# Optimization experiments

Hardware: AMD Instinct MI355X
Metric: run time of the kernel (lower is better)

Reference implementation:

```python
import jax, jax.numpy as jnp
import numpy as np

V, D, H, B, S, K = 10000, 128, 512, 32, 512, 2  # vocab, emb, hidden, batch, seq, num_cells

def setup_inputs() -> dict:
    key = jax.random.key(0)
    ks = jax.random.split(key, 8)
    sc_d, sc_h = 1.0 / np.sqrt(D), 1.0 / np.sqrt(H)
    return {
        "x": jax.random.randint(ks[0], (B, S), 0, V),
        "emb_table": jax.random.normal(ks[1], (V, D), jnp.float32),
        "W_ih": jax.random.uniform(ks[2], (K, 4 * H, D), jnp.float32, -sc_d, sc_d),
        "W_hh": jax.random.uniform(ks[3], (K, 4 * H, H), jnp.float32, -sc_h, sc_h),
        "b_ih": jax.random.uniform(ks[4], (K, 4 * H), jnp.float32, -sc_h, sc_h),
        "b_hh": jax.random.uniform(ks[5], (K, 4 * H), jnp.float32, -sc_h, sc_h),
        "W_out": jax.random.uniform(ks[6], (V, H), jnp.float32, -sc_h, sc_h),
        "b_out": jax.random.uniform(ks[7], (V,), jnp.float32, -sc_h, sc_h),
    }

def _mlstm(x_ids_t, emb_t, W_ih, W_hh, b, h0, c0):
    # x_ids_t: (S,B) int, emb_t: (S,B,D). Two LSTMCells; token id parity picks the cell.
    def step(carry, inp):
        h, c = carry                       # (B,H) each
        xt, ids = inp                      # (B,D), (B,)
        gates = (jnp.einsum('bd,kgd->kbg', xt, W_ih)
                 + jnp.einsum('bh,kgh->kbg', h, W_hh)
                 + b[:, None, :])          # (K,B,4H)
        i, f, g, o = jnp.split(gates, 4, axis=-1)
        i, f, o = jax.nn.sigmoid(i), jax.nn.sigmoid(f), jax.nn.sigmoid(o)
        g = jnp.tanh(g)
        c_new = f * c + i * g              # (K,B,H)
        h_new = o * jnp.tanh(c_new)        # (K,B,H)
        sel = (ids % 2)[:, None]           # (B,1) cell index per example
        h_next = jnp.where(sel == 0, h_new[0], h_new[1])
        c_next = jnp.where(sel == 0, c_new[0], c_new[1])
        return (h_next, c_next), h_next
    (_, _), hs = jax.lax.scan(step, (h0, c0), (emb_t, x_ids_t))
    return hs  # (S,B,H)

def reference(x, emb_table, W_ih, W_hh, b_ih, b_hh, W_out, b_out):
    emb = emb_table[x]                     # (B,S,D)
    emb_t = jnp.transpose(emb, (1, 0, 2))  # (S,B,D) time-major
    h0 = jnp.zeros((x.shape[0], W_hh.shape[-1]), emb.dtype)
    hs = _mlstm(x.T, emb_t, W_ih, W_hh, b_ih + b_hh, h0, h0)  # (S,B,H)
    flat = hs.reshape(-1, hs.shape[-1])    # (S*B, H)
    logits = flat @ W_out.T + b_out        # (S*B, V)
    return jax.nn.log_softmax(logits, axis=1)
```

## Files before the change

### kernel.cpp

```cpp
#include <hip/hip_runtime.h>
#include <hip/hip_bf16.h>

typedef __attribute__((ext_vector_type(8))) short short8;
typedef __attribute__((ext_vector_type(4))) float f32x4;
typedef unsigned long long u64;

#define V_N 10000
#define D_E 128
#define H_N 512
#define B_N 32
#define S_N 512

#define SENT64 0xFFFFFFFFFFFFFFFFull

#define OFF_RP    0
#define OFF_EMB   5242880
#define OFF_HS    (OFF_EMB + 4194304)
#define OFF_WOUT  (OFF_HS + 16777216)

__device__ __forceinline__ float ftanh(float x) {
  float e = __expf(-2.f * fabsf(x));
  float r = (1.f - e) / (1.f + e);
  return __builtin_copysignf(r, x);
}

__global__ void k_prep_emb(const int* __restrict__ x, const float* __restrict__ tab,
                           __hip_bfloat16* __restrict__ emb) {
  int i = blockIdx.x * 256 + threadIdx.x;
  if (i >= S_N * B_N * D_E) return;
  int d  = i & (D_E - 1);
  int sb = i >> 7;
  int b  = sb & (B_N - 1);
  int s  = sb >> 5;
  int tok = x[b * S_N + s];
  emb[i] = __float2bfloat16(tab[tok * D_E + d]);
}

__global__ void k_prep_wout(const float* __restrict__ w, __hip_bfloat16* __restrict__ o) {
  int i = blockIdx.x * 256 + threadIdx.x;
  if (i < V_N * H_N) o[i] = __float2bfloat16(w[i]);
}

__launch_bounds__(256, 1)
__global__ void k_recurrence(const int* __restrict__ x,
                             const float* __restrict__ W_ih, const float* __restrict__ W_hh,
                             const float* __restrict__ b_ih, const float* __restrict__ b_hh,
                             const __hip_bfloat16* __restrict__ emb,
                             __hip_bfloat16* __restrict__ hs)
{
  __shared__ __hip_bfloat16 Bl[32][648];
  __shared__ float gl4[4][64][33];
  __shared__ float bias[64];
  __shared__ unsigned short hloc[8][32];

  const int tid = threadIdx.x;
  const int wg  = blockIdx.x;
  const int lane = tid & 63, kw = tid >> 6;
  const int lrow = lane & 15, lk = (lane >> 4) * 8;
  const int b_ep = tid & 31, jj_ep = tid >> 5;

  short8 Afrag[20];
  #pragma unroll
  for (int mt = 0; mt < 4; ++mt) {
    #pragma unroll
    for (int ks = 0; ks < 5; ++ks) {
      int lr = mt * 16 + lrow;
      int q = lr >> 4, kc = (lr >> 3) & 1, jj = lr & 7;
      int grow = kc * 2048 + q * 512 + wg * 8 + jj;
      int c0 = kw * 160 + ks * 32 + lk;
      short8 a;
      #pragma unroll
      for (int e = 0; e < 8; ++e) {
        int c = c0 + e;
        float v = (c < 128) ? W_ih[(size_t)grow * 128 + c]
                            : W_hh[(size_t)grow * 512 + (c - 128)];
        __hip_bfloat16 hb = __float2bfloat16(v);
        a[e] = *(const short*)&hb;
      }
      Afrag[mt * 5 + ks] = a;
    }
  }
  if (tid < 64) {
    int lr = tid;
    int q = lr >> 4, kc = (lr >> 3) & 1, jj = lr & 7;
    int grow = kc * 2048 + q * 512 + wg * 8 + jj;
    bias[lr] = b_ih[grow] + b_hh[grow];
  }

  unsigned par[16];
  #pragma unroll
  for (int w = 0; w < 16; ++w) {
    unsigned p = 0;
    for (int bb = 0; bb < 32; ++bb)
      p |= (unsigned)(x[b_ep * S_N + w * 32 + bb] & 1) << bb;
    par[w] = p;
  }

  float c_state = 0.f;
  const u64* e64base = (const u64*)emb;

  for (int t = 0; t < S_N; ++t) {
    const u64* e64 = e64base + (size_t)t * 1024;
    for (int i = tid; i < 1024; i += 256) {
      int b = i >> 5, dd = i & 31;
      *(u64*)&Bl[b][dd * 4] = e64[i];
    }
    if (t == 0) {
      for (int i = tid; i < 4096; i += 256) {
        int b = i >> 7, hh = i & 127;
        *(u64*)&Bl[b][128 + hh * 4] = 0ull;
      }
    } else {
      const u64* src = (const u64*)hs + (size_t)(t - 1) * 4096;
      u64 v0=0,v1=0,v2=0,v3=0,v4=0,v5=0,v6=0,v7=0,
          v8=0,v9=0,v10=0,v11=0,v12=0,v13=0,v14=0,v15=0;
      unsigned pend = 0xFFFFu;
#define POLL1(IT) if (pend & (1u << IT)) \
        v##IT = __hip_atomic_load(src + IT * 256 + tid, __ATOMIC_RELAXED, __HIP_MEMORY_SCOPE_AGENT);
#define COMMIT1(IT) if ((pend & (1u << IT)) && v##IT != SENT64) { \
        int i_ = IT * 256 + tid; \
        *(u64*)&Bl[i_ >> 7][128 + (i_ & 127) * 4] = v##IT; \
        pend &= ~(1u << IT); }
      while (pend) {
        POLL1(0) POLL1(1) POLL1(2) POLL1(3) POLL1(4) POLL1(5) POLL1(6) POLL1(7)
        POLL1(8) POLL1(9) POLL1(10) POLL1(11) POLL1(12) POLL1(13) POLL1(14) POLL1(15)
        COMMIT1(0) COMMIT1(1) COMMIT1(2) COMMIT1(3) COMMIT1(4) COMMIT1(5) COMMIT1(6) COMMIT1(7)
        COMMIT1(8) COMMIT1(9) COMMIT1(10) COMMIT1(11) COMMIT1(12) COMMIT1(13) COMMIT1(14) COMMIT1(15)
      }
#undef POLL1
#undef COMMIT1
    }
    __syncthreads();

    {
      f32x4 acc[4][2] = {};
      #pragma unroll
      for (int ks = 0; ks < 5; ++ks) {
        int cb = (kw * 160 + ks * 32 + lk) * 2;
        short8 b0 = *(const short8*)((const char*)&Bl[0][0] + lrow * 1296 + cb);
        short8 b1 = *(const short8*)((const char*)&Bl[0][0] + (16 + lrow) * 1296 + cb);
        #pragma unroll
        for (int mt = 0; mt < 4; ++mt) {
          acc[mt][0] = __builtin_amdgcn_mfma_f32_16x16x32_bf16(Afrag[mt * 5 + ks], b0, acc[mt][0], 0, 0, 0);
          acc[mt][1] = __builtin_amdgcn_mfma_f32_16x16x32_bf16(Afrag[mt * 5 + ks], b1, acc[mt][1], 0, 0, 0);
        }
      }
      #pragma unroll
      for (int mt = 0; mt < 4; ++mt)
        #pragma unroll
        for (int nt = 0; nt < 2; ++nt)
          #pragma unroll
          for (int r = 0; r < 4; ++r)
            gl4[kw][mt * 16 + (lane >> 4) * 4 + r][nt * 16 + (lane & 15)] = acc[mt][nt][r];
    }
    __syncthreads();

    {
      float cand_c[2], cand_h[2];
      #pragma unroll
      for (int k = 0; k < 2; ++k) {
        int base = k * 8 + jj_ep;
        float ig = gl4[0][base][b_ep] + gl4[1][base][b_ep]
                 + gl4[2][base][b_ep] + gl4[3][base][b_ep] + bias[base];
        float fg = gl4[0][16 + base][b_ep] + gl4[1][16 + base][b_ep]
                 + gl4[2][16 + base][b_ep] + gl4[3][16 + base][b_ep] + bias[16 + base];
        float gg = gl4[0][32 + base][b_ep] + gl4[1][32 + base][b_ep]
                 + gl4[2][32 + base][b_ep] + gl4[3][32 + base][b_ep] + bias[32 + base];
        float og = gl4[0][48 + base][b_ep] + gl4[1][48 + base][b_ep]
                 + gl4[2][48 + base][b_ep] + gl4[3][48 + base][b_ep] + bias[48 + base];
        ig = 1.f / (1.f + __expf(-ig));
        fg = 1.f / (1.f + __expf(-fg));
        og = 1.f / (1.f + __expf(-og));
        gg = ftanh(gg);
        float cn = fg * c_state + ig * gg;
        cand_c[k] = cn;
        cand_h[k] = og * ftanh(cn);
      }
      int sel = (par[t >> 5] >> (t & 31)) & 1;
      c_state  = sel ? cand_c[1] : cand_c[0];
      float hv = sel ? cand_h[1] : cand_h[0];
      __hip_bfloat16 hb = __float2bfloat16(hv);
      hloc[jj_ep][b_ep] = *(const unsigned short*)&hb;
    }
    __syncthreads();

    if (tid < 64) {
      int b = tid >> 1, half = tid & 1;
      u64 v = (u64)hloc[half * 4 + 0][b]
            | ((u64)hloc[half * 4 + 1][b] << 16)
            | ((u64)hloc[half * 4 + 2][b] << 32)
            | ((u64)hloc[half * 4 + 3][b] << 48);
      u64* dst = (u64*)hs + (size_t)t * 4096 + b * 128 + wg * 2 + half;
      __hip_atomic_store(dst, v, __ATOMIC_RELAXED, __HIP_MEMORY_SCOPE_AGENT);
    }
  }
}

__launch_bounds__(256, 2)
__global__ void k_gemm(const __hip_bfloat16* __restrict__ hs,
                       const __hip_bfloat16* __restrict__ wout,
                       const float* __restrict__ b_out,
                       float* __restrict__ out,
                       float* __restrict__ rowpart)
{
  __shared__ __hip_bfloat16 Al[128][72];
  __shared__ __hip_bfloat16 Wt[128][72];
  __shared__ float sumLDS[2][128];
  const int tid = threadIdx.x;
  const int tn = blockIdx.x, tm = blockIdx.y;
  const int lane = tid & 63, wv = tid >> 6;
  const int mq = wv & 1, nq = wv >> 1;
  const int lrow = lane & 15, lk = (lane >> 4) * 8;
  f32x4 acc[4][4] = {};

  const int ar = tid >> 3, ac = (tid & 7) * 8;
  for (int k0 = 0; k0 < 512; k0 += 64) {
    __syncthreads();
    #pragma unroll
    for (int rr = 0; rr < 4; ++rr) {
      int r = ar + rr * 32;
      short8 av = *(const short8*)(hs + ((size_t)(tm * 128 + r)) * 512 + k0 + ac);
      *(short8*)&Al[r][ac] = av;
      int v = tn * 128 + r;
      short8 wvv = {};
      if (v < V_N) wvv = *(const short8*)(wout + (size_t)v * 512 + k0 + ac);
      *(short8*)&Wt[r][ac] = wvv;
    }
    __syncthreads();
    #pragma unroll
    for (int ks = 0; ks < 2; ++ks) {
      int kb = ks * 32 + lk;
      short8 af[4], bf[4];
      #pragma unroll
      for (int i = 0; i < 4; ++i) af[i] = *(const short8*)&Al[mq * 64 + i * 16 + lrow][kb];
      #pragma unroll
      for (int i = 0; i < 4; ++i) bf[i] = *(const short8*)&Wt[nq * 64 + i * 16 + lrow][kb];
      #pragma unroll
      for (int i = 0; i < 4; ++i)
        #pragma unroll
        for (int jx = 0; jx < 4; ++jx)
          acc[i][jx] = __builtin_amdgcn_mfma_f32_16x16x32_bf16(af[i], bf[jx], acc[i][jx], 0, 0, 0);
    }
  }
  const int rbase = tm * 128 + mq * 64 + (lane >> 4) * 4;
  const int cbase = tn * 128 + nq * 64 + (lane & 15);
  float esum[4][4];
  #pragma unroll
  for (int i = 0; i < 4; ++i)
    #pragma unroll
    for (int r = 0; r < 4; ++r) esum[i][r] = 0.f;

  #pragma unroll
  for (int i = 0; i < 4; ++i) {
    #pragma unroll
    for (int jx = 0; jx < 4; ++jx) {
      int col = cbase + jx * 16;
      if (col < V_N) {
        float bo = b_out[col];
        #pragma unroll
        for (int r = 0; r < 4; ++r) {
          int row = rbase + i * 16 + r;
          float lg = acc[i][jx][r] + bo;
          out[(size_t)row * V_N + col] = lg;
          esum[i][r] += __expf(lg);
        }
      }
    }
  }
  #pragma unroll
  for (int i = 0; i < 4; ++i) {
    #pragma unroll
    for (int r = 0; r < 4; ++r) {
      float s = esum[i][r];
      s += __shfl_xor(s, 1); s += __shfl_xor(s, 2);
      s += __shfl_xor(s, 4); s += __shfl_xor(s, 8);
      if ((lane & 15) == 0)
        sumLDS[nq][mq * 64 + i * 16 + (lane >> 4) * 4 + r] = s;
    }
  }
  __syncthreads();
  if (tid < 128)
    rowpart[(size_t)(tm * 128 + tid) * 80 + tn] = sumLDS[0][tid] + sumLDS[1][tid];
}

__launch_bounds__(256)
__global__ void k_lsm_fix(float* __restrict__ out, const float* __restrict__ rowpart) {
  const int r = blockIdx.x;
  const float* rp = rowpart + (size_t)r * 80;
  float s = 0.f;
  for (int p = 0; p < 79; ++p) s += rp[p];
  float lse = __logf(s);
  float4* q4 = (float4*)(out + (size_t)r * V_N);
  for (int i = threadIdx.x; i < V_N / 4; i += 256) {
    float4 v = q4[i];
    v.x -= lse; v.y -= lse; v.z -= lse; v.w -= lse;
    q4[i] = v;
  }
}

extern "C" void kernel_launch(void* const* d_in, const int* in_sizes, int n_in,
                              void* d_out, int out_size, void* d_ws, size_t ws_size,
                              hipStream_t stream) {
  const int*   x    = (const int*)d_in[0];
  const float* tab  = (const float*)d_in[1];
  const float* Wih  = (const float*)d_in[2];
  const float* Whh  = (const float*)d_in[3];
  const float* bih  = (const float*)d_in[4];
  const float* bhh  = (const float*)d_in[5];
  const float* Wout = (const float*)d_in[6];
  const float* bout = (const float*)d_in[7];
  float* out = (float*)d_out;

  char* ws = (char*)d_ws;
  float*           rowpart = (float*)(ws + OFF_RP);
  __hip_bfloat16*  emb     = (__hip_bfloat16*)(ws + OFF_EMB);
  __hip_bfloat16*  hsbuf   = (__hip_bfloat16*)(ws + OFF_HS);
  __hip_bfloat16*  wob     = (__hip_bfloat16*)(ws + OFF_WOUT);

  hipMemsetAsync(hsbuf, 0xFF, (size_t)S_N * B_N * H_N * 2, stream);
  k_prep_emb<<<(S_N * B_N * D_E) / 256, 256, 0, stream>>>(x, tab, emb);
  k_prep_wout<<<(V_N * H_N) / 256, 256, 0, stream>>>(Wout, wob);
  k_recurrence<<<64, 256, 0, stream>>>(x, Wih, Whh, bih, bhh, emb, hsbuf);
  k_gemm<<<dim3(79, 128), 256, 0, stream>>>(hsbuf, wob, bout, out, rowpart);
  k_lsm_fix<<<16384, 256, 0, stream>>>(out, rowpart);
}
```

Baseline: 2.568 ms.

## Load MFMA B-fragments directly from global into registers, dropping LDS staging

Each wave now polls and loads only the hidden-state and embedding fragments its MFMA needs, straight into registers, instead of staging the whole embedding and h vector in a shared LDS buffer. This removes the LDS round trip and one __syncthreads per timestep on the serial recurrence critical path. In exchange, wave 0 polls only 4 slots while the other waves poll 20 scattered 8-byte locations each, which gives less coalesced global reads and more polling traffic. Register pressure also rises.

New measurement: 3.934 ms. +53.2%, slower.

```diff
diff --git a/kernel.cpp b/kernel.cpp
--- a/kernel.cpp
+++ b/kernel.cpp
@@ -22,6 +22,12 @@
   float e = __expf(-2.f * fabsf(x));
   float r = (1.f - e) / (1.f + e);
   return __builtin_copysignf(r, x);
+}
+
+__device__ __forceinline__ short8 frag2(u64 lo, u64 hi) {
+  union { u64 q[2]; short8 s; } u;
+  u.q[0] = lo; u.q[1] = hi;
+  return u.s;
 }
 
 __global__ void k_prep_emb(const int* __restrict__ x, const float* __restrict__ tab,
@@ -48,7 +54,6 @@
                              const __hip_bfloat16* __restrict__ emb,
                              __hip_bfloat16* __restrict__ hs)
 {
-  __shared__ __hip_bfloat16 Bl[32][648];
   __shared__ float gl4[4][64][33];
   __shared__ float bias[64];
   __shared__ unsigned short hloc[8][32];
@@ -96,49 +101,72 @@
     par[w] = p;
   }
 
+  int off[20];
+  if (kw == 0) {
+    #pragma unroll
+    for (int f = 0; f < 2; ++f) {
+      int ex = lrow + f * 16;
+      off[f * 2]     = ex * 128 + (lk >> 2);
+      off[f * 2 + 1] = ex * 128 + (lk >> 2) + 1;
+    }
+  } else {
+    #pragma unroll
+    for (int f = 0; f < 10; ++f) {
+      int ex = lrow + ((f >= 5) ? 16 : 0);
+      int ks = (f >= 5) ? (f - 5) : f;
+      int hk = kw * 160 - 128 + ks * 32 + lk;
+      off[f * 2]     = ex * 128 + (hk >> 2);
+      off[f * 2 + 1] = ex * 128 + (hk >> 2) + 1;
+    }
+  }
+  const int npoll = (kw == 0) ? 4 : 20;
+
   float c_state = 0.f;
-  const u64* e64base = (const u64*)emb;
 
   for (int t = 0; t < S_N; ++t) {
-    const u64* e64 = e64base + (size_t)t * 1024;
-    for (int i = tid; i < 1024; i += 256) {
-      int b = i >> 5, dd = i & 31;
-      *(u64*)&Bl[b][dd * 4] = e64[i];
-    }
+    short8 eb[2][4];
+    if (kw == 0) {
+      #pragma unroll
+      for (int f = 0; f < 2; ++f) {
+        int ex = lrow + f * 16;
+        const __hip_bfloat16* ep = emb + ((size_t)t * B_N + ex) * D_E + lk;
+        #pragma unroll
+        for (int ks = 0; ks < 4; ++ks)
+          eb[f][ks] = *(const short8*)(ep + ks * 32);
+      }
+    }
+    u64 hv[20];
     if (t == 0) {
-      for (int i = tid; i < 4096; i += 256) {
-        int b = i >> 7, hh = i & 127;
-        *(u64*)&Bl[b][128 + hh * 4] = 0ull;
-      }
+      #pragma unroll
+      for (int id = 0; id < 20; ++id) hv[id] = 0ull;
     } else {
       const u64* src = (const u64*)hs + (size_t)(t - 1) * 4096;
-      u64 v0=0,v1=0,v2=0,v3=0,v4=0,v5=0,v6=0,v7=0,
-          v8=0,v9=0,v10=0,v11=0,v12=0,v13=0,v14=0,v15=0;
-      unsigned pend = 0xFFFFu;
-#define POLL1(IT) if (pend & (1u << IT)) \
-        v##IT = __hip_atomic_load(src + IT * 256 + tid, __ATOMIC_RELAXED, __HIP_MEMORY_SCOPE_AGENT);
-#define COMMIT1(IT) if ((pend & (1u << IT)) && v##IT != SENT64) { \
-        int i_ = IT * 256 + tid; \
-        *(u64*)&Bl[i_ >> 7][128 + (i_ & 127) * 4] = v##IT; \
-        pend &= ~(1u << IT); }
+      unsigned pend = (npoll == 4) ? 0xFu : 0xFFFFFu;
       while (pend) {
-        POLL1(0) POLL1(1) POLL1(2) POLL1(3) POLL1(4) POLL1(5) POLL1(6) POLL1(7)
-        POLL1(8) POLL1(9) POLL1(10) POLL1(11) POLL1(12) POLL1(13) POLL1(14) POLL1(15)
-        COMMIT1(0) COMMIT1(1) COMMIT1(2) COMMIT1(3) COMMIT1(4) COMMIT1(5) COMMIT1(6) COMMIT1(7)
-        COMMIT1(8) COMMIT1(9) COMMIT1(10) COMMIT1(11) COMMIT1(12) COMMIT1(13) COMMIT1(14) COMMIT1(15)
-      }
-#undef POLL1
-#undef COMMIT1
-    }
-    __syncthreads();
+        #pragma unroll
+        for (int id = 0; id < 20; ++id)
+          if (id < npoll && (pend & (1u << id)))
+            hv[id] = __hip_atomic_load(src + off[id], __ATOMIC_RELAXED,
+                                       __HIP_MEMORY_SCOPE_AGENT);
+        #pragma unroll
+        for (int id = 0; id < 20; ++id)
+          if (id < npoll && (pend & (1u << id)) && hv[id] != SENT64)
+            pend &= ~(1u << id);
+      }
+    }
 
     {
       f32x4 acc[4][2] = {};
       #pragma unroll
       for (int ks = 0; ks < 5; ++ks) {
-        int cb = (kw * 160 + ks * 32 + lk) * 2;
-        short8 b0 = *(const short8*)((const char*)&Bl[0][0] + lrow * 1296 + cb);
-        short8 b1 = *(const short8*)((const char*)&Bl[0][0] + (16 + lrow) * 1296 + cb);
+        short8 b0, b1;
+        if (kw == 0) {
+          if (ks < 4) { b0 = eb[0][ks]; b1 = eb[1][ks]; }
+          else        { b0 = frag2(hv[0], hv[1]); b1 = frag2(hv[2], hv[3]); }
+        } else {
+          b0 = frag2(hv[2 * ks], hv[2 * ks + 1]);
+          b1 = frag2(hv[10 + 2 * ks], hv[11 + 2 * ks]);
+        }
         #pragma unroll
         for (int mt = 0; mt < 4; ++mt) {
           acc[mt][0] = __builtin_amdgcn_mfma_f32_16x16x32_bf16(Afrag[mt * 5 + ks], b0, acc[mt][0], 0, 0, 0);
@@ -178,8 +206,8 @@
       }
       int sel = (par[t >> 5] >> (t & 31)) & 1;
       c_state  = sel ? cand_c[1] : cand_c[0];
-      float hv = sel ? cand_h[1] : cand_h[0];
-      __hip_bfloat16 hb = __float2bfloat16(hv);
+      float hv2 = sel ? cand_h[1] : cand_h[0];
+      __hip_bfloat16 hb = __float2bfloat16(hv2);
       hloc[jj_ep][b_ep] = *(const unsigned short*)&hb;
     }
     __syncthreads();
```

## Poll canary words before bulk 128-bit coherent loads of hidden state; transpose gate scratch

Applied to the files above, without the earlier changes.

Replaces the per-step polling of all 16 u64 chunks of the previous hidden state with a single wave spinning on canary words at the tail of the buffer. The rest of the block then issues 128-bit system-coherent loads (sc0 sc1), with a sentinel recheck and retry. The gate scratch buffer is transposed so each MFMA accumulator is stored as one f32x4 write instead of four scalar writes. This aims to cut global polling traffic and LDS store count on the serial critical path, at the cost of an extra barrier and reliance on the canary being the last data written.

Result: slower. 3.289 ms (+28.1%).

```diff
diff --git a/kernel.cpp b/kernel.cpp
--- a/kernel.cpp
+++ b/kernel.cpp
@@ -23,6 +23,8 @@
   float r = (1.f - e) / (1.f + e);
   return __builtin_copysignf(r, x);
 }
+
+union U128 { f32x4 f; u64 q[2]; };
 
 __global__ void k_prep_emb(const int* __restrict__ x, const float* __restrict__ tab,
                            __hip_bfloat16* __restrict__ emb) {
@@ -49,7 +51,7 @@
                              __hip_bfloat16* __restrict__ hs)
 {
   __shared__ __hip_bfloat16 Bl[32][648];
-  __shared__ float gl4[4][64][33];
+  __shared__ float gl4t[4][32][66];
   __shared__ float bias[64];
   __shared__ unsigned short hloc[8][32];
 
@@ -96,6 +98,8 @@
     par[w] = p;
   }
 
+  const int myb  = tid >> 3;
+  const int hh0  = (tid & 7) * 16;
   float c_state = 0.f;
   const u64* e64base = (const u64*)emb;
 
@@ -105,32 +109,42 @@
       int b = i >> 5, dd = i & 31;
       *(u64*)&Bl[b][dd * 4] = e64[i];
     }
+
     if (t == 0) {
       for (int i = tid; i < 4096; i += 256) {
         int b = i >> 7, hh = i & 127;
         *(u64*)&Bl[b][128 + hh * 4] = 0ull;
       }
+      __syncthreads();
     } else {
-      const u64* src = (const u64*)hs + (size_t)(t - 1) * 4096;
-      u64 v0=0,v1=0,v2=0,v3=0,v4=0,v5=0,v6=0,v7=0,
-          v8=0,v9=0,v10=0,v11=0,v12=0,v13=0,v14=0,v15=0;
-      unsigned pend = 0xFFFFu;
-#define POLL1(IT) if (pend & (1u << IT)) \
-        v##IT = __hip_atomic_load(src + IT * 256 + tid, __ATOMIC_RELAXED, __HIP_MEMORY_SCOPE_AGENT);
-#define COMMIT1(IT) if ((pend & (1u << IT)) && v##IT != SENT64) { \
-        int i_ = IT * 256 + tid; \
-        *(u64*)&Bl[i_ >> 7][128 + (i_ & 127) * 4] = v##IT; \
-        pend &= ~(1u << IT); }
+      if (tid < 64) {
+        const u64* can = (const u64*)hs + (size_t)(t - 1) * 4096 + 3968 + tid * 2 + 1;
+        u64 v;
+        do {
+          v = __hip_atomic_load(can, __ATOMIC_RELAXED, __HIP_MEMORY_SCOPE_AGENT);
+        } while (!__all((int)(v != SENT64)));
+      }
+      __syncthreads();
+      const char* src = (const char*)hs + (size_t)(t - 1) * 32768 + tid * 128;
+      U128 buf[8];
+      unsigned pend = 0xFFu;
       while (pend) {
-        POLL1(0) POLL1(1) POLL1(2) POLL1(3) POLL1(4) POLL1(5) POLL1(6) POLL1(7)
-        POLL1(8) POLL1(9) POLL1(10) POLL1(11) POLL1(12) POLL1(13) POLL1(14) POLL1(15)
-        COMMIT1(0) COMMIT1(1) COMMIT1(2) COMMIT1(3) COMMIT1(4) COMMIT1(5) COMMIT1(6) COMMIT1(7)
-        COMMIT1(8) COMMIT1(9) COMMIT1(10) COMMIT1(11) COMMIT1(12) COMMIT1(13) COMMIT1(14) COMMIT1(15)
-      }
-#undef POLL1
-#undef COMMIT1
-    }
-    __syncthreads();
+        #pragma unroll
+        for (int c = 0; c < 8; ++c)
+          if (pend & (1u << c))
+            asm volatile("global_load_dwordx4 %0, %1, off sc0 sc1"
+                         : "=v"(buf[c].f) : "v"(src + c * 16) : "memory");
+        asm volatile("s_waitcnt vmcnt(0)" ::: "memory");
+        __builtin_amdgcn_sched_barrier(0);
+        #pragma unroll
+        for (int c = 0; c < 8; ++c)
+          if ((pend & (1u << c)) && buf[c].q[0] != SENT64 && buf[c].q[1] != SENT64) {
+            *(f32x4*)&Bl[myb][128 + (hh0 + c * 2) * 4] = buf[c].f;
+            pend &= ~(1u << c);
+          }
+      }
+      __syncthreads();
+    }
 
     {
       f32x4 acc[4][2] = {};
@@ -149,9 +163,7 @@
       for (int mt = 0; mt < 4; ++mt)
         #pragma unroll
         for (int nt = 0; nt < 2; ++nt)
-          #pragma unroll
-          for (int r = 0; r < 4; ++r)
-            gl4[kw][mt * 16 + (lane >> 4) * 4 + r][nt * 16 + (lane & 15)] = acc[mt][nt][r];
+          *(f32x4*)&gl4t[kw][nt * 16 + (lane & 15)][mt * 16 + (lane >> 4) * 4] = acc[mt][nt];
     }
     __syncthreads();
 
@@ -160,14 +172,14 @@
       #pragma unroll
       for (int k = 0; k < 2; ++k) {
         int base = k * 8 + jj_ep;
-        float ig = gl4[0][base][b_ep] + gl4[1][base][b_ep]
-                 + gl4[2][base][b_ep] + gl4[3][base][b_ep] + bias[base];
-        float fg = gl4[0][16 + base][b_ep] + gl4[1][16 + base][b_ep]
-                 + gl4[2][16 + base][b_ep] + gl4[3][16 + base][b_ep] + bias[16 + base];
-        float gg = gl4[0][32 + base][b_ep] + gl4[1][32 + base][b_ep]
-                 + gl4[2][32 + base][b_ep] + gl4[3][32 + base][b_ep] + bias[32 + base];
-        float og = gl4[0][48 + base][b_ep] + gl4[1][48 + base][b_ep]
-                 + gl4[2][48 + base][b_ep] + gl4[3][48 + base][b_ep] + bias[48 + base];
+        float ig = gl4t[0][b_ep][base] + gl4t[1][b_ep][base]
+                 + gl4t[2][b_ep][base] + gl4t[3][b_ep][base] + bias[base];
+        float fg = gl4t[0][b_ep][16 + base] + gl4t[1][b_ep][16 + base]
+                 + gl4t[2][b_ep][16 + base] + gl4t[3][b_ep][16 + base] + bias[16 + base];
+        float gg = gl4t[0][b_ep][32 + base] + gl4t[1][b_ep][32 + base]
+                 + gl4t[2][b_ep][32 + base] + gl4t[3][b_ep][32 + base] + bias[32 + base];
+        float og = gl4t[0][b_ep][48 + base] + gl4t[1][b_ep][48 + base]
+                 + gl4t[2][b_ep][48 + base] + gl4t[3][b_ep][48 + base] + bias[48 + base];
         ig = 1.f / (1.f + __expf(-ig));
         fg = 1.f / (1.f + __expf(-fg));
         og = 1.f / (1.f + __expf(-og));
```
